# Performance work log

Measured on AMD Instinct MI355X. Metric: run time of the kernel, lower is better.

The kernel has to match this reference:

```python
import jax, jax.numpy as jnp
import numpy as np

C = 192
DCT = 7
EPS = 1e-5
LOW_X = [0,0,1,1,0,2,2,1,2,0,3,4,0,1,3,0,1,2,3,4,5,0,1,2,3,4,5,6,1,2,3,4]
LOW_Y = [0,1,0,1,2,0,1,2,2,3,0,0,4,3,1,5,4,3,2,1,0,6,5,4,3,2,1,0,6,5,4,3]


def _dct_basis():
    # basis[i, tx, ty] = bf(tx, ux_i, DCT) * bf(ty, vy_i, DCT)
    t = jnp.arange(DCT, dtype=jnp.float32)
    fx = jnp.array(LOW_X, dtype=jnp.float32)  # mapper scale = dct_h//7 = 1
    fy = jnp.array(LOW_Y, dtype=jnp.float32)
    def bf(freq):
        r = jnp.cos(jnp.pi * freq[:, None] * (t[None, :] + 0.5) / DCT) / jnp.sqrt(jnp.float32(DCT))
        return jnp.where(freq[:, None] == 0, r, r * jnp.sqrt(jnp.float32(2.0)))
    bx, by = bf(fx), bf(fy)  # [32, 7] each
    return bx[:, :, None] * by[:, None, :]  # [32, 7, 7]


def reference(x, wg1, bn2_g, bn2_b, bn2_m, bn2_v, wg2, bg2, beta, w1d, b1d, bn1_g, bn1_b, bn1_m, bn1_v):
    n, c, h, w = x.shape
    # gate: 1x1 conv -> BN2d (eval) -> ReLU -> global avg pool -> 1x1 conv
    g = jnp.einsum('nchw,oc->nohw', x, wg1)
    g = (g - bn2_m[None, :, None, None]) * (bn2_g / jnp.sqrt(bn2_v + EPS))[None, :, None, None] + bn2_b[None, :, None, None]
    g = jax.nn.relu(g).mean(axis=(2, 3))          # [n, 32]
    xg = g @ wg2.T + bg2                           # [n, 32]
    xg = jax.nn.relu(jnp.tanh(xg)) + beta          # gate_ac + beta
    # data-dependent channel partition from batch element 0 (torch uses .item() -> detached)
    xg0 = jax.lax.stop_gradient(xg[0])
    s = xg0.sum()
    p_mid = jnp.round(xg0[:31] / s * c)            # param[1..31]
    param = jnp.concatenate([jnp.zeros(1, jnp.float32), p_mid,
                             (jnp.float32(c) - p_mid.sum())[None]])  # [33]
    # build DCT filter: slice param[i]:param[i+1] gets basis i, later i overwrites
    ch = jnp.arange(c, dtype=jnp.float32)
    basis = _dct_basis()                           # [32, 7, 7]
    filt = jnp.zeros((c, DCT, DCT), jnp.float32)
    for i in range(32):
        m = (ch >= param[i]) & (ch < param[i + 1])
        filt = jnp.where(m[:, None, None], basis[i], filt)
    xp = x.reshape(n, c, DCT, h // DCT, DCT, w // DCT).mean(axis=(3, 5))
    y = jnp.sum(xp * filt[None], axis=(2, 3))      # [n, c] weighted spatial pooling
    # Conv1d(c, c, k=3, pad=1) on length-1 sequence: only center tap w1d[:, :, 1]
    y = y @ w1d[:, :, 1].T + b1d
    y = (y - bn1_m) * (bn1_g / jnp.sqrt(bn1_v + EPS)) + bn1_b
    y = jax.nn.relu(y)
    return x * y[:, :, None, None] + x


def setup_inputs() -> dict:
    key = jax.random.key(0)
    ks = jax.random.split(key, 16)
    n, h, w = 64, 56, 56
    return {
        'x':     jax.random.normal(ks[0], (n, C, h, w), jnp.float32),
        'wg1':   jax.random.normal(ks[1], (32, C), jnp.float32) * (2.0 / C) ** 0.5,
        'bn2_g': jax.random.uniform(ks[2], (32,), jnp.float32, 0.8, 1.2),
        'bn2_b': jax.random.normal(ks[3], (32,), jnp.float32) * 0.1,
        'bn2_m': jax.random.normal(ks[4], (32,), jnp.float32) * 0.1,
        'bn2_v': jax.random.uniform(ks[5], (32,), jnp.float32, 0.5, 1.5),
        'wg2':   jax.random.normal(ks[6], (32, 32), jnp.float32) * (2.0 / 32) ** 0.5,
        'bg2':   jax.random.normal(ks[7], (32,), jnp.float32) * 0.1,
        'beta':  jax.random.uniform(ks[8], (1,), jnp.float32, 0.05, 0.25),
        'w1d':   jax.random.normal(ks[9], (C, C, 3), jnp.float32) * (2.0 / (3 * C)) ** 0.5,
        'b1d':   jax.random.normal(ks[10], (C,), jnp.float32) * 0.1,
        'bn1_g': jax.random.uniform(ks[11], (C,), jnp.float32, 0.8, 1.2),
        'bn1_b': jax.random.normal(ks[12], (C,), jnp.float32) * 0.1,
        'bn1_m': jax.random.normal(ks[13], (C,), jnp.float32) * 0.1,
        'bn1_v': jax.random.uniform(ks[14], (C,), jnp.float32, 0.5, 1.5),
    }
```

## Files before the change

### kernel.cpp

```cpp
#include <hip/hip_runtime.h>
#include <hip/hip_bf16.h>
#include <math.h>

#define CCH 192
#define EPS 1e-5f

typedef float vfloat4 __attribute__((ext_vector_type(4)));

__device__ __constant__ int d_LOWX[32] = {0,0,1,1,0,2,2,1,2,0,3,4,0,1,3,0,1,2,3,4,5,0,1,2,3,4,5,6,1,2,3,4};
__device__ __constant__ int d_LOWY[32] = {0,1,0,1,2,0,1,2,2,3,0,0,4,3,1,5,4,3,2,1,0,6,5,4,3,2,1,0,6,5,4,3};

#define GLOAD4(dst, addr) \
  asm volatile("global_load_dwordx4 %0, %1, off" : "=v"(dst) : "v"(addr))
#define GLOAD1(dst, addr) \
  asm volatile("global_load_dword %0, %1, off" : "=v"(dst) : "v"(addr))
#define VMWAIT0() do { \
  asm volatile("s_waitcnt vmcnt(0)" ::: "memory"); \
  __builtin_amdgcn_sched_barrier(0); \
} while (0)

__global__ __launch_bounds__(256) void fused_pre_kernel(
    const float* __restrict__ x, const float* __restrict__ w1d,
    const float* __restrict__ wg1,
    const float* __restrict__ bn2_g, const float* __restrict__ bn2_b,
    const float* __restrict__ bn2_m, const float* __restrict__ bn2_v,
    float* __restrict__ xp, float* __restrict__ wt, float* __restrict__ partial) {
  __shared__ float smem[4 * 49];
  const int b = blockIdx.x;
  const int t = threadIdx.x;
  if (b >= 200) {
    const int pb = b - 200;
    const int n = pb / 48, c0 = (pb % 48) * 4;
    const int wv = t >> 6, l = t & 63;
    const int c = c0 + wv;
    const bool act = l < 56;
    const int lidx = act ? l : 0;
    const vfloat4* xv = (const vfloat4*)(x + (size_t)(n * CCH + c) * 3136);
    vfloat4 va[7], vb[7];
#pragma unroll
    for (int g = 0; g < 7; ++g) {
      GLOAD4(va[g], xv + g * 112 + lidx);
      GLOAD4(vb[g], xv + g * 112 + 56 + lidx);
    }
    VMWAIT0();
    float as[7];
#pragma unroll
    for (int g = 0; g < 7; ++g) {
      float s = (va[g].x + va[g].y + va[g].z + va[g].w) +
                (vb[g].x + vb[g].y + vb[g].z + vb[g].w);
      as[g] = act ? s : 0.f;
    }
#pragma unroll
    for (int g = 0; g < 7; ++g) {
      float a = as[g] + __shfl_xor(as[g], 1);
      a += __shfl(a, l + 28);
      a += __shfl(a, l + 14);
      if (act && l < 14 && (l & 1) == 0)
        smem[wv * 49 + g * 7 + (l >> 1)] = a;
    }
    __syncthreads();
    if (t < 196) xp[((size_t)n * CCH + c0) * 49 + t] = smem[t] * (1.f / 64.f);
  } else if (b >= 56) {
    const int i = (b - 56) * 256 + t;
    const int cc = i / CCH, k = i - cc * CCH;
    wt[k * CCH + cc] = w1d[cc * (CCH * 3) + 3 * k + 1];
  } else {
    const int h = b;
    const int wv = t >> 6, w = t & 63;
    float acc[8];
#pragma unroll
    for (int o = 0; o < 8; ++o) acc[o] = 0.f;
    const float* xrow = x + h * 56;
    for (int cc0 = 0; cc0 < CCH; cc0 += 8) {
      float xq[8];
#pragma unroll
      for (int j = 0; j < 8; ++j)
        GLOAD1(xq[j], xrow + (size_t)(cc0 + j) * 3136 + ((w < 56) ? w : 0));
      VMWAIT0();
#pragma unroll
      for (int j = 0; j < 8; ++j) {
        float xvv = (w < 56) ? xq[j] : 0.f;
#pragma unroll
        for (int o = 0; o < 8; ++o)
          acc[o] += xvv * wg1[(wv * 8 + o) * CCH + cc0 + j];
      }
    }
#pragma unroll
    for (int o = 0; o < 8; ++o) {
      const int oo = wv * 8 + o;
      float sc = bn2_g[oo] * rsqrtf(bn2_v[oo] + EPS);
      float v = acc[o] * sc + (bn2_b[oo] - bn2_m[oo] * sc);
      v = (w < 56) ? fmaxf(v, 0.f) : 0.f;
#pragma unroll
      for (int s = 1; s < 64; s <<= 1) v += __shfl_xor(v, s);
      if (w == 0) partial[h * 32 + oo] = v;
    }
  }
}

__global__ __launch_bounds__(256) void scale_kernel(
    const float* __restrict__ partial, const float* __restrict__ wg2,
    const float* __restrict__ bg2, const float* __restrict__ beta,
    const float* __restrict__ xp, const float* __restrict__ wt,
    const float* __restrict__ b1d,
    const float* __restrict__ bn1_g, const float* __restrict__ bn1_b,
    const float* __restrict__ bn1_m, const float* __restrict__ bn1_v,
    float* __restrict__ scale) {
  __shared__ float gm[32];
  __shared__ float xg[32];
  __shared__ float param[33];
  __shared__ float Btab[49];
  __shared__ float yl[CCH];
  const int n = blockIdx.x, t = threadIdx.x;
  if (t < 32) {
    float s = 0.f;
    for (int hh = 0; hh < 56; ++hh) s += partial[hh * 32 + t];
    gm[t] = s * (1.f / 3136.f);
  }
  if (t < 49) {
    int f = t / 7, tt = t % 7;
    float r = cosf(3.14159265358979323846f * (float)f * ((float)tt + 0.5f) / 7.f) * rsqrtf(7.f);
    Btab[t] = (f == 0) ? r : r * sqrtf(2.f);
  }
  __syncthreads();
  if (t < 32) {
    float a = bg2[t];
    for (int k = 0; k < 32; ++k) a += gm[k] * wg2[t * 32 + k];
    xg[t] = fmaxf(tanhf(a), 0.f) + beta[0];
  }
  __syncthreads();
  if (t == 0) {
    float s = 0.f;
    for (int k = 0; k < 32; ++k) s += xg[k];
    float psum = 0.f;
    param[0] = 0.f;
    for (int i = 0; i < 31; ++i) {
      float p = rintf(xg[i] / s * (float)CCH);
      param[i + 1] = p;
      psum += p;
    }
    param[32] = (float)CCH - psum;
  }
  __syncthreads();
  if (t < CCH) {
    int bi = -1;
    float cf = (float)t;
    for (int i = 0; i < 32; ++i)
      if (cf >= param[i] && cf < param[i + 1]) bi = i;
    int fx = (bi >= 0) ? d_LOWX[bi] : 0;
    int fy = (bi >= 0) ? d_LOWY[bi] : 0;
    const float* xc = xp + ((size_t)n * CCH + t) * 49;
    float s = 0.f;
    for (int cell = 0; cell < 49; ++cell) {
      int a = cell / 7, bb = cell - a * 7;
      float w = Btab[fx * 7 + a] * Btab[fy * 7 + bb];
      s += xc[cell] * ((bi >= 0) ? w : 0.f);
    }
    yl[t] = s;
  }
  __syncthreads();
  if (t < CCH) {
    float acc = b1d[t];
#pragma unroll 8
    for (int k = 0; k < CCH; ++k) acc += yl[k] * wt[k * CCH + t];
    float sc = bn1_g[t] * rsqrtf(bn1_v[t] + EPS);
    float v = (acc - bn1_m[t]) * sc + bn1_b[t];
    scale[n * CCH + t] = 1.f + fmaxf(v, 0.f);
  }
}

__global__ __launch_bounds__(256) void apply_kernel(
    const float* __restrict__ x, const float* __restrict__ scale,
    float* __restrict__ out) {
  const int base = blockIdx.x * 2048 + threadIdx.x;
  const vfloat4* __restrict__ xv = (const vfloat4*)x;
  vfloat4* __restrict__ ov = (vfloat4*)out;
  vfloat4 vv[8];
  float sj[8];
#pragma unroll
  for (int k = 0; k < 8; ++k) {
    const int f = base + k * 256;
    GLOAD4(vv[k], xv + f);
    GLOAD1(sj[k], scale + f / 784);
  }
  VMWAIT0();
#pragma unroll
  for (int k = 0; k < 8; ++k) {
    const int f = base + k * 256;
    ov[f] = vv[k] * sj[k];
  }
}

extern "C" void kernel_launch(void* const* d_in, const int* in_sizes, int n_in,
                              void* d_out, int out_size, void* d_ws, size_t ws_size,
                              hipStream_t stream) {
  const float* x     = (const float*)d_in[0];
  const float* wg1   = (const float*)d_in[1];
  const float* bn2_g = (const float*)d_in[2];
  const float* bn2_b = (const float*)d_in[3];
  const float* bn2_m = (const float*)d_in[4];
  const float* bn2_v = (const float*)d_in[5];
  const float* wg2   = (const float*)d_in[6];
  const float* bg2   = (const float*)d_in[7];
  const float* beta  = (const float*)d_in[8];
  const float* w1d   = (const float*)d_in[9];
  const float* b1d   = (const float*)d_in[10];
  const float* bn1_g = (const float*)d_in[11];
  const float* bn1_b = (const float*)d_in[12];
  const float* bn1_m = (const float*)d_in[13];
  const float* bn1_v = (const float*)d_in[14];
  float* out = (float*)d_out;

  float* ws      = (float*)d_ws;
  float* partial = ws;
  float* filt    = partial + 1792;
  float* wt      = filt + 9408;
  float* xp      = wt + 36864;
  float* scale   = xp + 602112;

  fused_pre_kernel<<<3272, 256, 0, stream>>>(x, w1d, wg1, bn2_g, bn2_b, bn2_m, bn2_v,
                                             xp, wt, partial);
  scale_kernel<<<64, 256, 0, stream>>>(partial, wg2, bg2, beta, xp, wt, b1d,
                                       bn1_g, bn1_b, bn1_m, bn1_v, scale);
  apply_kernel<<<4704, 256, 0, stream>>>(x, scale, out);
}
```

Before: 345.2 us.

## Process four channel groups per pooling block with double-buffered loads

Each pooling block now covers 16 channels (four groups of four) instead of four. It double-buffers the vector loads with partial vmcnt waits, so the next group's loads overlap the current group's reduction. Results go straight to global memory from the shuffle lanes, dropping the shared-memory staging and the barrier, and the grid shrinks from 3272 to 968 blocks. The cost is higher register pressure (28 float4 buffers) and fewer blocks, which may lower occupancy for a memory-bound pass.

```diff
diff --git a/kernel.cpp b/kernel.cpp
--- a/kernel.cpp
+++ b/kernel.cpp
@@ -14,9 +14,30 @@
   asm volatile("global_load_dwordx4 %0, %1, off" : "=v"(dst) : "v"(addr))
 #define GLOAD1(dst, addr) \
   asm volatile("global_load_dword %0, %1, off" : "=v"(dst) : "v"(addr))
-#define VMWAIT0() do { \
-  asm volatile("s_waitcnt vmcnt(0)" ::: "memory"); \
+#define VMWAIT(n) do { \
+  asm volatile("s_waitcnt vmcnt(" #n ")" ::: "memory"); \
   __builtin_amdgcn_sched_barrier(0); \
+} while (0)
+
+#define ISSUE(buf, base) do { \
+  _Pragma("unroll") \
+  for (int g = 0; g < 7; ++g) { \
+    GLOAD4(buf[2 * g],     (base) + g * 112 + lidx); \
+    GLOAD4(buf[2 * g + 1], (base) + g * 112 + 56 + lidx); \
+  } \
+} while (0)
+
+#define REDUCE(buf, res) do { \
+  _Pragma("unroll") \
+  for (int g = 0; g < 7; ++g) { \
+    float s = (buf[2*g].x + buf[2*g].y + buf[2*g].z + buf[2*g].w) + \
+              (buf[2*g+1].x + buf[2*g+1].y + buf[2*g+1].z + buf[2*g+1].w); \
+    s = act ? s : 0.f; \
+    float a = s + __shfl_xor(s, 1); \
+    a += __shfl(a, l + 28); \
+    a += __shfl(a, l + 14); \
+    res[g] = a; \
+  } \
 } while (0)
 
 __global__ __launch_bounds__(256) void fused_pre_kernel(
@@ -25,41 +46,48 @@
     const float* __restrict__ bn2_g, const float* __restrict__ bn2_b,
     const float* __restrict__ bn2_m, const float* __restrict__ bn2_v,
     float* __restrict__ xp, float* __restrict__ wt, float* __restrict__ partial) {
-  __shared__ float smem[4 * 49];
   const int b = blockIdx.x;
   const int t = threadIdx.x;
   if (b >= 200) {
-    const int pb = b - 200;
-    const int n = pb / 48, c0 = (pb % 48) * 4;
+    const int ub = b - 200;
+    const int n = ub / 12;
+    const int q0 = (ub % 12) * 4;
     const int wv = t >> 6, l = t & 63;
-    const int c = c0 + wv;
     const bool act = l < 56;
     const int lidx = act ? l : 0;
-    const vfloat4* xv = (const vfloat4*)(x + (size_t)(n * CCH + c) * 3136);
-    vfloat4 va[7], vb[7];
-#pragma unroll
-    for (int g = 0; g < 7; ++g) {
-      GLOAD4(va[g], xv + g * 112 + lidx);
-      GLOAD4(vb[g], xv + g * 112 + 56 + lidx);
-    }
-    VMWAIT0();
-    float as[7];
-#pragma unroll
-    for (int g = 0; g < 7; ++g) {
-      float s = (va[g].x + va[g].y + va[g].z + va[g].w) +
-                (vb[g].x + vb[g].y + vb[g].z + vb[g].w);
-      as[g] = act ? s : 0.f;
-    }
-#pragma unroll
-    for (int g = 0; g < 7; ++g) {
-      float a = as[g] + __shfl_xor(as[g], 1);
-      a += __shfl(a, l + 28);
-      a += __shfl(a, l + 14);
-      if (act && l < 14 && (l & 1) == 0)
-        smem[wv * 49 + g * 7 + (l >> 1)] = a;
-    }
-    __syncthreads();
-    if (t < 196) xp[((size_t)n * CCH + c0) * 49 + t] = smem[t] * (1.f / 64.f);
+    const vfloat4* xb = (const vfloat4*)(x + (size_t)n * CCH * 3136 + (size_t)wv * 3136);
+    const vfloat4* base0 = xb + (size_t)(q0 + 0) * 4 * 784;
+    const vfloat4* base1 = xb + (size_t)(q0 + 1) * 4 * 784;
+    const vfloat4* base2 = xb + (size_t)(q0 + 2) * 4 * 784;
+    const vfloat4* base3 = xb + (size_t)(q0 + 3) * 4 * 784;
+    vfloat4 A[14], B[14];
+    float r0[7], r1[7], r2[7], r3[7];
+    ISSUE(A, base0);
+    ISSUE(B, base1);
+    VMWAIT(14);
+    REDUCE(A, r0);
+    ISSUE(A, base2);
+    VMWAIT(14);
+    REDUCE(B, r1);
+    ISSUE(B, base3);
+    VMWAIT(14);
+    REDUCE(A, r2);
+    VMWAIT(0);
+    REDUCE(B, r3);
+    if (act && l < 14 && (l & 1) == 0) {
+      const int cb = l >> 1;
+      float* d0 = xp + ((size_t)n * CCH + (q0 + 0) * 4 + wv) * 49 + cb;
+      float* d1 = xp + ((size_t)n * CCH + (q0 + 1) * 4 + wv) * 49 + cb;
+      float* d2 = xp + ((size_t)n * CCH + (q0 + 2) * 4 + wv) * 49 + cb;
+      float* d3 = xp + ((size_t)n * CCH + (q0 + 3) * 4 + wv) * 49 + cb;
+#pragma unroll
+      for (int g = 0; g < 7; ++g) {
+        d0[g * 7] = r0[g] * (1.f / 64.f);
+        d1[g * 7] = r1[g] * (1.f / 64.f);
+        d2[g * 7] = r2[g] * (1.f / 64.f);
+        d3[g * 7] = r3[g] * (1.f / 64.f);
+      }
+    }
   } else if (b >= 56) {
     const int i = (b - 56) * 256 + t;
     const int cc = i / CCH, k = i - cc * CCH;
@@ -76,7 +104,7 @@
 #pragma unroll
       for (int j = 0; j < 8; ++j)
         GLOAD1(xq[j], xrow + (size_t)(cc0 + j) * 3136 + ((w < 56) ? w : 0));
-      VMWAIT0();
+      VMWAIT(0);
 #pragma unroll
       for (int j = 0; j < 8; ++j) {
         float xvv = (w < 56) ? xq[j] : 0.f;
@@ -183,7 +211,7 @@
     GLOAD4(vv[k], xv + f);
     GLOAD1(sj[k], scale + f / 784);
   }
-  VMWAIT0();
+  VMWAIT(0);
 #pragma unroll
   for (int k = 0; k < 8; ++k) {
     const int f = base + k * 256;
@@ -218,8 +246,8 @@
   float* xp      = wt + 36864;
   float* scale   = xp + 602112;
 
-  fused_pre_kernel<<<3272, 256, 0, stream>>>(x, w1d, wg1, bn2_g, bn2_b, bn2_m, bn2_v,
-                                             xp, wt, partial);
+  fused_pre_kernel<<<968, 256, 0, stream>>>(x, w1d, wg1, bn2_g, bn2_b, bn2_m, bn2_v,
+                                            xp, wt, partial);
   scale_kernel<<<64, 256, 0, stream>>>(partial, wg2, bg2, beta, xp, wt, b1d,
                                        bn1_g, bn1_b, bn1_m, bn1_v, scale);
   apply_kernel<<<4704, 256, 0, stream>>>(x, scale, out);
```

New measurement: 340.2 us. No clear change (-1.4%).
